# Performance work log

Hardware: AMD Instinct MI355X
Metric: run time of the kernel (lower is better)

The kernel has to match this reference:

```python
import jax, jax.numpy as jnp
import numpy as np
from jax.ops import segment_sum

N_NODES = 100_000
N_EDGES = 3_200_000
IN_DIM = 128
HID1, HID2, OUT = 32, 16, 1
N_GRAPHS = 512


def gcn_conv(x, src, dst, W, b, n_nodes):
    """PyG GCNConv: add self-loops, symmetric deg^{-1/2} norm, scatter-add, bias."""
    h = x @ W  # [N, out]
    loop = jnp.arange(n_nodes, dtype=src.dtype)
    s = jnp.concatenate([src, loop])
    d = jnp.concatenate([dst, loop])
    deg = segment_sum(jnp.ones_like(d, dtype=h.dtype), d, num_segments=n_nodes)
    dinv = jax.lax.rsqrt(jnp.maximum(deg, 1.0))  # deg >= 1 due to self-loops
    norm = dinv[s] * dinv[d]  # [E+N]
    msg = h[s] * norm[:, None]  # gather + scale
    out = segment_sum(msg, d, num_segments=n_nodes)  # scatter-add to dst
    return out + b


def setup_inputs() -> dict:
    key = jax.random.key(0)
    ks = jax.random.split(key, 9)
    x = jax.random.normal(ks[0], (N_NODES, IN_DIM), dtype=jnp.float32)
    edge_index = jax.random.randint(ks[1], (2, N_EDGES), 0, N_NODES, dtype=jnp.int64)
    batch = jnp.sort(jax.random.randint(ks[2], (N_NODES,), 0, N_GRAPHS, dtype=jnp.int64))
    W1 = jax.random.normal(ks[3], (IN_DIM, HID1), dtype=jnp.float32) * 0.1
    b1 = jnp.zeros((HID1,), dtype=jnp.float32)
    W2 = jax.random.normal(ks[4], (HID1, HID2), dtype=jnp.float32) * 0.1
    b2 = jnp.zeros((HID2,), dtype=jnp.float32)
    W3 = jax.random.normal(ks[5], (HID2, OUT), dtype=jnp.float32) * 0.1
    b3 = jnp.zeros((OUT,), dtype=jnp.float32)
    return {"x": x, "edge_index": edge_index, "batch": batch,
            "W1": W1, "b1": b1, "W2": W2, "b2": b2, "W3": W3, "b3": b3}


def reference(x, edge_index, batch, W1, b1, W2, b2, W3, b3):
    src, dst = edge_index[0], edge_index[1]
    n = x.shape[0]
    h = jax.nn.relu(gcn_conv(x, src, dst, W1, b1, n))
    h = jax.nn.relu(gcn_conv(h, src, dst, W2, b2, n))
    # global_mean_pool: segment mean over graph ids
    summed = segment_sum(h, batch, num_segments=N_GRAPHS)  # [G, HID2]
    counts = segment_sum(jnp.ones((n,), dtype=h.dtype), batch, num_segments=N_GRAPHS)
    pooled = summed / jnp.maximum(counts, 1.0)[:, None]
    return pooled @ W3 + b3  # [G, 1]
```

## Files before the change

### kernel.cpp

```cpp
#include <hip/hip_runtime.h>
#include <hip/hip_fp16.h>

#define NN 100000
#define NE 3200000
#define NG 512
#define IND 128
#define H1D 32
#define H2D 16
#define BSH 7
#define BN  128
#define NB  782
#define TILE 8192
#define NBF 391
#define CAP 5120

#define O_DINV   0u
#define O_ROW    100352u
#define O_REND   200704u
#define O_GCUR   301056u
#define O_GSUM   302080u
#define O_M1H    302592u
#define O_M2H    1902592u
#define O_CSRB   2702592u
#define O_CSR    6706432u

__global__ __launch_bounds__(256) void k_init(int* gcur, float* gsum) {
    int i = blockIdx.x * 256 + threadIdx.x;
    if (i < 1024) gcur[i] = i * CAP;
    if (i < NG) gsum[i] = 0.f;
}

__global__ __launch_bounds__(256) void k_prep1(const int* __restrict__ src,
                                               const int* __restrict__ dst,
                                               int* __restrict__ gcur,
                                               unsigned* __restrict__ csrb,
                                               const float* __restrict__ x,
                                               const float* __restrict__ W1,
                                               __half* __restrict__ m1h) {
    __shared__ __align__(16) unsigned char smem[30208];
    int t = threadIdx.x;
    if (blockIdx.x < NBF) {
        unsigned short* se16 = (unsigned short*)smem;
        int* lc   = (int*)(smem + 16384);
        int* lofs = (int*)(smem + 19584);
        int* lcur = (int*)(smem + 22784);
        int* gb   = (int*)(smem + 25984);
        int* sp   = (int*)(smem + 29184);
        for (int i = t; i < NB; i += 256) lc[i] = 0;
        __syncthreads();
        int base = blockIdx.x * TILE;
        int end = min(base + TILE, NE);
        int n = end - base;
        int n4 = n >> 2;
        const int4* dst4 = (const int4*)(dst + base);
        for (int u = t; u < n4; u += 256) {
            int4 v = dst4[u];
            atomicAdd(&lc[v.x >> BSH], 1);
            atomicAdd(&lc[v.y >> BSH], 1);
            atomicAdd(&lc[v.z >> BSH], 1);
            atomicAdd(&lc[v.w >> BSH], 1);
        }
        __syncthreads();
        int b0 = 4 * t;
        int c0 = (b0     < NB) ? lc[b0]     : 0;
        int c1 = (b0 + 1 < NB) ? lc[b0 + 1] : 0;
        int c2 = (b0 + 2 < NB) ? lc[b0 + 2] : 0;
        int c3 = (b0 + 3 < NB) ? lc[b0 + 3] : 0;
        int s4 = c0 + c1 + c2 + c3;
        sp[t] = s4;
        __syncthreads();
        for (int off = 1; off < 256; off <<= 1) {
            int v = (t >= off) ? sp[t - off] : 0;
            __syncthreads();
            sp[t] += v;
            __syncthreads();
        }
        int excl = sp[t] - s4;
        if (b0     < NB) { lofs[b0]     = excl;                lcur[b0]     = excl; }
        if (b0 + 1 < NB) { lofs[b0 + 1] = excl + c0;           lcur[b0 + 1] = excl + c0; }
        if (b0 + 2 < NB) { lofs[b0 + 2] = excl + c0 + c1;      lcur[b0 + 2] = excl + c0 + c1; }
        if (b0 + 3 < NB) { lofs[b0 + 3] = excl + c0 + c1 + c2; lcur[b0 + 3] = excl + c0 + c1 + c2; }
        __syncthreads();
        for (int i = t; i < NB; i += 256) {
            int c = lc[i];
            gb[i] = c ? atomicAdd(&gcur[i], c) : 0;
        }
        __syncthreads();
        for (int u = t; u < n4; u += 256) {
            int4 v = dst4[u];
            int uu = u * 4;
            int b, p;
            b = v.x >> BSH; p = atomicAdd(&lcur[b], 1); se16[p] = (unsigned short)(uu);
            b = v.y >> BSH; p = atomicAdd(&lcur[b], 1); se16[p] = (unsigned short)(uu + 1);
            b = v.z >> BSH; p = atomicAdd(&lcur[b], 1); se16[p] = (unsigned short)(uu + 2);
            b = v.w >> BSH; p = atomicAdd(&lcur[b], 1); se16[p] = (unsigned short)(uu + 3);
        }
        __syncthreads();
        for (int i = t; i < n; i += 256) {
            int u = se16[i];
            int d = dst[base + u];
            int s = src[base + u];
            int b = d >> BSH;
            int pos = gb[b] + (i - lofs[b]);
            csrb[pos] = (unsigned)s | ((unsigned)(d & (BN - 1)) << 17);
        }
    } else {
        float* sWt = (float*)smem;
        float* sX  = (float*)(smem + 16896);
        int gbk = blockIdx.x - NBF;
        for (int idx = t; idx < IND * H1D; idx += 256) {
            int i = idx >> 5, k = idx & 31;
            sWt[k * 132 + i] = W1[idx];
        }
        const float4* x4 = (const float4*)(x + (size_t)gbk * 16 * IND);
        ((float4*)sX)[t] = x4[t];
        ((float4*)sX)[t + 256] = x4[t + 256];
        __syncthreads();
        int r = t >> 5, k = t & 31;
        float a0 = 0.f, a1 = 0.f;
#pragma unroll
        for (int i = 0; i < IND; i += 4) {
            float4 w = *(const float4*)&sWt[k * 132 + i];
            float4 p = *(const float4*)&sX[r * IND + i];
            float4 s = *(const float4*)&sX[(r + 8) * IND + i];
            a0 += p.x * w.x + p.y * w.y + p.z * w.z + p.w * w.w;
            a1 += s.x * w.x + s.y * w.y + s.z * w.z + s.w * w.w;
        }
        int n0 = gbk * 16 + r;
        m1h[(size_t)n0 * 32 + k] = __float2half(a0);
        m1h[(size_t)(n0 + 8) * 32 + k] = __float2half(a1);
    }
}

__global__ __launch_bounds__(256) void k_reorder(const unsigned* __restrict__ csrb,
                                                 const int* __restrict__ gcur,
                                                 int* __restrict__ rowstart,
                                                 int* __restrict__ rowend,
                                                 float* __restrict__ dinv,
                                                 int* __restrict__ csr,
                                                 __half* __restrict__ m1h) {
    __shared__ int so[CAP];
    __shared__ int h[BN], cur[BN];
    __shared__ float sdv[BN];
    int t = threadIdx.x;
    int b = blockIdx.x;
    int base = b * CAP;
    int cnt = gcur[b] - base;
    if (t < BN) h[t] = 0;
    __syncthreads();
    for (int i = t; i < cnt; i += 256)
        atomicAdd(&h[csrb[base + i] >> 17], 1);
    __syncthreads();
    int deg = (t < BN) ? h[t] : 0;
    for (int off = 1; off < BN; off <<= 1) {
        int v = (t < BN && t >= off) ? h[t - off] : 0;
        __syncthreads();
        if (t < BN) h[t] += v;
        __syncthreads();
    }
    int excl = (t < BN) ? (h[t] - deg) : 0;
    if (t < BN) cur[t] = excl;
    int node = (b << BSH) + t;
    if (t < BN) {
        float dv = 1.0f / sqrtf((float)(deg + 1));
        sdv[t] = dv;
        if (node < NN) {
            rowstart[node] = base + excl;
            rowend[node]   = base + excl + deg;
            dinv[node] = dv;
        }
    }
    __syncthreads();
    for (int i = t; i < cnt; i += 256) {
        unsigned p = csrb[base + i];
        int pos = atomicAdd(&cur[p >> 17], 1);
        so[pos] = (int)(p & 0x1FFFF);
    }
    __syncthreads();
    for (int i = t; i < cnt; i += 256)
        csr[base + i] = so[i];
    int nn = min(BN, NN - (b << BSH));
    __half2* mrow = (__half2*)(m1h + (size_t)(b << BSH) * 32);
    for (int idx = t; idx < nn * 16; idx += 256) {
        float dv = sdv[idx >> 4];
        float2 f = __half22float2(mrow[idx]);
        mrow[idx] = __floats2half2_rn(f.x * dv, f.y * dv);
    }
}

__device__ __forceinline__ void h8_acc(const float4& r, float* a) {
    const __half2* h = (const __half2*)&r;
    float2 f0 = __half22float2(h[0]);
    float2 f1 = __half22float2(h[1]);
    float2 f2 = __half22float2(h[2]);
    float2 f3 = __half22float2(h[3]);
    a[0] += f0.x; a[1] += f0.y; a[2] += f1.x; a[3] += f1.y;
    a[4] += f2.x; a[5] += f2.y; a[6] += f3.x; a[7] += f3.y;
}

__global__ __launch_bounds__(256) void k_agg1(const __half* __restrict__ m1h,
                                              const float* __restrict__ dinv,
                                              const int* __restrict__ rowstart,
                                              const int* __restrict__ rowend,
                                              const int* __restrict__ csr,
                                              const float* __restrict__ b1,
                                              const float* __restrict__ W2,
                                              __half* __restrict__ m2h) {
    int t = threadIdx.x;
    int lane = t & 63;
    int j = (lane >> 2) & 7;
    int q = lane & 3;
    int d = (blockIdx.x * 256 + t) >> 5;
    int beg = rowstart[d], end = rowend[d];
    float dv = dinv[d];
    const float4* m4 = (const float4*)m1h;
    float4 selfr = m4[(size_t)d * 4 + q];
    float a[8] = {0.f, 0.f, 0.f, 0.f, 0.f, 0.f, 0.f, 0.f};
    int i = beg + j;
    for (; i + 24 < end; i += 32) {
        int s0 = csr[i], s1 = csr[i + 8], s2 = csr[i + 16], s3 = csr[i + 24];
        float4 A = m4[(size_t)s0 * 4 + q];
        float4 B = m4[(size_t)s1 * 4 + q];
        float4 C = m4[(size_t)s2 * 4 + q];
        float4 D = m4[(size_t)s3 * 4 + q];
        h8_acc(A, a); h8_acc(B, a); h8_acc(C, a); h8_acc(D, a);
    }
    for (; i + 8 < end; i += 16) {
        int s0 = csr[i], s1 = csr[i + 8];
        float4 A = m4[(size_t)s0 * 4 + q];
        float4 B = m4[(size_t)s1 * 4 + q];
        h8_acc(A, a); h8_acc(B, a);
    }
    if (i < end) {
        int s0 = csr[i];
        float4 A = m4[(size_t)s0 * 4 + q];
        h8_acc(A, a);
    }
#pragma unroll
    for (int m = 4; m <= 16; m <<= 1) {
#pragma unroll
        for (int e = 0; e < 8; ++e) a[e] += __shfl_xor(a[e], m);
    }
    float sf[8] = {0.f, 0.f, 0.f, 0.f, 0.f, 0.f, 0.f, 0.f};
    h8_acc(selfr, sf);
    float4 ba = ((const float4*)b1)[q * 2];
    float4 bb = ((const float4*)b1)[q * 2 + 1];
    float bias[8] = {ba.x, ba.y, ba.z, ba.w, bb.x, bb.y, bb.z, bb.w};
    float v[8];
#pragma unroll
    for (int e = 0; e < 8; ++e)
        v[e] = fmaxf((a[e] + sf[e]) * dv + bias[e], 0.f);
    const float2* W2_2 = (const float2*)W2;
    float p0 = 0.f, p1 = 0.f;
#pragma unroll
    for (int e = 0; e < 8; ++e) {
        float2 w = W2_2[(q * 8 + e) * 8 + j];
        p0 += v[e] * w.x;
        p1 += v[e] * w.y;
    }
    p0 += __shfl_xor(p0, 1); p1 += __shfl_xor(p1, 1);
    p0 += __shfl_xor(p0, 2); p1 += __shfl_xor(p1, 2);
    if (q == 0)
        *(__half2*)&m2h[(size_t)d * 16 + 2 * j] = __floats2half2_rn(p0 * dv, p1 * dv);
}

__global__ __launch_bounds__(256) void k_agg2(const __half* __restrict__ m2h,
                                              const float* __restrict__ dinv,
                                              const int* __restrict__ rowstart,
                                              const int* __restrict__ rowend,
                                              const int* __restrict__ csr,
                                              const float* __restrict__ b2,
                                              const float* __restrict__ W3,
                                              const int* __restrict__ batch,
                                              float* __restrict__ gsum) {
    __shared__ float bsum[8];
    __shared__ int   bg[8];
    int t = threadIdx.x;
    int lane = t & 63;
    int j = (lane >> 1) & 15;
    int q = lane & 1;
    int d = (blockIdx.x * 256 + t) >> 5;
    int beg = rowstart[d], end = rowend[d];
    float dv = dinv[d];
    const float4* m4 = (const float4*)m2h;
    float4 selfr = m4[(size_t)d * 2 + q];
    float a[8] = {0.f, 0.f, 0.f, 0.f, 0.f, 0.f, 0.f, 0.f};
    int i = beg + j;
    for (; i + 48 < end; i += 64) {
        int s0 = csr[i], s1 = csr[i + 16], s2 = csr[i + 32], s3 = csr[i + 48];
        float4 A = m4[(size_t)s0 * 2 + q];
        float4 B = m4[(size_t)s1 * 2 + q];
        float4 C = m4[(size_t)s2 * 2 + q];
        float4 D = m4[(size_t)s3 * 2 + q];
        h8_acc(A, a); h8_acc(B, a); h8_acc(C, a); h8_acc(D, a);
    }
    for (; i + 16 < end; i += 32) {
        int s0 = csr[i], s1 = csr[i + 16];
        float4 A = m4[(size_t)s0 * 2 + q];
        float4 B = m4[(size_t)s1 * 2 + q];
        h8_acc(A, a); h8_acc(B, a);
    }
    if (i < end) {
        int s0 = csr[i];
        float4 A = m4[(size_t)s0 * 2 + q];
        h8_acc(A, a);
    }
#pragma unroll
    for (int m = 2; m <= 16; m <<= 1) {
#pragma unroll
        for (int e = 0; e < 8; ++e) a[e] += __shfl_xor(a[e], m);
    }
    float sf[8] = {0.f, 0.f, 0.f, 0.f, 0.f, 0.f, 0.f, 0.f};
    h8_acc(selfr, sf);
    float4 ba = ((const float4*)b2)[q * 2];
    float4 bb = ((const float4*)b2)[q * 2 + 1];
    float4 wa = ((const float4*)W3)[q * 2];
    float4 wb = ((const float4*)W3)[q * 2 + 1];
    float bias[8] = {ba.x, ba.y, ba.z, ba.w, bb.x, bb.y, bb.z, bb.w};
    float w3[8]   = {wa.x, wa.y, wa.z, wa.w, wb.x, wb.y, wb.z, wb.w};
    float partial = 0.f;
#pragma unroll
    for (int e = 0; e < 8; ++e) {
        float v = fmaxf((a[e] + sf[e]) * dv + bias[e], 0.f);
        partial += v * w3[e];
    }
    partial += __shfl_xor(partial, 1);
    int hw = t >> 5;
    if ((lane & 31) == 0) { bg[hw] = batch[d]; bsum[hw] = partial; }
    __syncthreads();
    if (t == 0) {
        float s = bsum[0]; int g = bg[0];
#pragma unroll
        for (int u = 1; u < 8; ++u) {
            if (bg[u] == g) s += bsum[u];
            else { atomicAdd(&gsum[g], s); g = bg[u]; s = bsum[u]; }
        }
        atomicAdd(&gsum[g], s);
    }
}

__global__ __launch_bounds__(256) void k_final(const float* __restrict__ gsum,
                                               const int* __restrict__ batch,
                                               const float* __restrict__ b3,
                                               float* __restrict__ out) {
    int g = blockIdx.x * 256 + threadIdx.x;
    if (g >= NG) return;
    int lo = 0, hi = NN;
    while (lo < hi) { int mid = (lo + hi) >> 1; if (batch[mid] < g) lo = mid + 1; else hi = mid; }
    int lo2 = lo, hi2 = NN;
    while (lo2 < hi2) { int mid = (lo2 + hi2) >> 1; if (batch[mid] < g + 1) lo2 = mid + 1; else hi2 = mid; }
    out[g] = gsum[g] / fmaxf((float)(lo2 - lo), 1.0f) + b3[0];
}

extern "C" void kernel_launch(void* const* d_in, const int* in_sizes, int n_in,
                              void* d_out, int out_size, void* d_ws, size_t ws_size,
                              hipStream_t stream) {
    const float* x     = (const float*)d_in[0];
    const int*   src   = (const int*)d_in[1];
    const int*   dst   = src + NE;
    const int*   batch = (const int*)d_in[2];
    const float* W1 = (const float*)d_in[3];
    const float* b1 = (const float*)d_in[4];
    const float* W2 = (const float*)d_in[5];
    const float* b2 = (const float*)d_in[6];
    const float* W3 = (const float*)d_in[7];
    const float* b3 = (const float*)d_in[8];
    float* out = (float*)d_out;

    float* ws = (float*)d_ws;
    float*    dinv     = ws + O_DINV;
    int*      rowstart = (int*)(ws + O_ROW);
    int*      rowend   = (int*)(ws + O_REND);
    int*      gcur     = (int*)(ws + O_GCUR);
    float*    gsum     = ws + O_GSUM;
    __half*   m1h      = (__half*)(ws + O_M1H);
    __half*   m2h      = (__half*)(ws + O_M2H);
    unsigned* csrb     = (unsigned*)(ws + O_CSRB);
    int*      csr      = (int*)(ws + O_CSR);

    k_init   <<<4, 256, 0, stream>>>(gcur, gsum);
    k_prep1  <<<NBF + NN / 16, 256, 0, stream>>>(src, dst, gcur, csrb, x, W1, m1h);
    k_reorder<<<NB, 256, 0, stream>>>(csrb, gcur, rowstart, rowend, dinv, csr, m1h);
    k_agg1   <<<NN / 8, 256, 0, stream>>>(m1h, dinv, rowstart, rowend, csr, b1, W2, m2h);
    k_agg2   <<<NN / 8, 256, 0, stream>>>(m2h, dinv, rowstart, rowend, csr, b2, W3, batch, gsum);
    k_final  <<<2, 256, 0, stream>>>(gsum, batch, b3, out);
}
```

Measured before the change: 297.7 us.

## Split reorder blocks in half and fuse final pooling into agg2 via last-block ticket

k_reorder now runs two blocks per bucket, each scattering and writing the CSR entries and scaling m1h rows for only half of the 128 destination nodes. Both blocks redundantly histogram and scan the whole bucket. k_final is removed: k_agg2 takes an atomic ticket after a threadfence, and the last block to finish computes the per-graph means and writes the output. This adds parallelism to the reorder stage and removes one launch, at the cost of repeated histogram work and a serialized tail in the last agg2 block.

After: 511.6 us. +71.9%, slower.

```diff
diff --git a/kernel.cpp b/kernel.cpp
--- a/kernel.cpp
+++ b/kernel.cpp
@@ -19,15 +19,17 @@
 #define O_REND   200704u
 #define O_GCUR   301056u
 #define O_GSUM   302080u
-#define O_M1H    302592u
-#define O_M2H    1902592u
-#define O_CSRB   2702592u
-#define O_CSR    6706432u
-
-__global__ __launch_bounds__(256) void k_init(int* gcur, float* gsum) {
+#define O_TICK   302592u
+#define O_M1H    302720u
+#define O_M2H    1902720u
+#define O_CSRB   2702720u
+#define O_CSR    6706560u
+
+__global__ __launch_bounds__(256) void k_init(int* gcur, float* gsum, int* tick) {
     int i = blockIdx.x * 256 + threadIdx.x;
     if (i < 1024) gcur[i] = i * CAP;
     if (i < NG) gsum[i] = 0.f;
+    if (i == 0) tick[0] = 0;
 }
 
 __global__ __launch_bounds__(256) void k_prep1(const int* __restrict__ src,
@@ -143,7 +145,8 @@
     __shared__ int h[BN], cur[BN];
     __shared__ float sdv[BN];
     int t = threadIdx.x;
-    int b = blockIdx.x;
+    int b = blockIdx.x >> 1;
+    int half = blockIdx.x & 1;
     int base = b * CAP;
     int cnt = gcur[b] - base;
     if (t < BN) h[t] = 0;
@@ -161,7 +164,7 @@
     int excl = (t < BN) ? (h[t] - deg) : 0;
     if (t < BN) cur[t] = excl;
     int node = (b << BSH) + t;
-    if (t < BN) {
+    if (t < BN && (t >> 6) == half) {
         float dv = 1.0f / sqrtf((float)(deg + 1));
         sdv[t] = dv;
         if (node < NN) {
@@ -173,18 +176,26 @@
     __syncthreads();
     for (int i = t; i < cnt; i += 256) {
         unsigned p = csrb[base + i];
-        int pos = atomicAdd(&cur[p >> 17], 1);
-        so[pos] = (int)(p & 0x1FFFF);
-    }
-    __syncthreads();
-    for (int i = t; i < cnt; i += 256)
+        int dl = p >> 17;
+        if ((dl >> 6) == half) {
+            int pos = atomicAdd(&cur[dl], 1);
+            so[pos] = (int)(p & 0x1FFFF);
+        }
+    }
+    __syncthreads();
+    int s0 = half ? h[63] : 0;
+    int e0 = half ? cnt : h[63];
+    for (int i = s0 + t; i < e0; i += 256)
         csr[base + i] = so[i];
-    int nn = min(BN, NN - (b << BSH));
-    __half2* mrow = (__half2*)(m1h + (size_t)(b << BSH) * 32);
-    for (int idx = t; idx < nn * 16; idx += 256) {
-        float dv = sdv[idx >> 4];
-        float2 f = __half22float2(mrow[idx]);
-        mrow[idx] = __floats2half2_rn(f.x * dv, f.y * dv);
+    int nbase = (b << BSH) + half * 64;
+    int nn = min(64, NN - nbase);
+    if (nn > 0) {
+        __half2* mrow = (__half2*)(m1h + (size_t)nbase * 32);
+        for (int idx = t; idx < nn * 16; idx += 256) {
+            float dv = sdv[half * 64 + (idx >> 4)];
+            float2 f = __half22float2(mrow[idx]);
+            mrow[idx] = __floats2half2_rn(f.x * dv, f.y * dv);
+        }
     }
 }
 
@@ -272,9 +283,13 @@
                                               const float* __restrict__ b2,
                                               const float* __restrict__ W3,
                                               const int* __restrict__ batch,
-                                              float* __restrict__ gsum) {
+                                              float* __restrict__ gsum,
+                                              int* __restrict__ tick,
+                                              const float* __restrict__ b3,
+                                              float* __restrict__ out) {
     __shared__ float bsum[8];
     __shared__ int   bg[8];
+    __shared__ int   slast;
     int t = threadIdx.x;
     int lane = t & 63;
     int j = (lane >> 1) & 15;
@@ -336,20 +351,20 @@
             else { atomicAdd(&gsum[g], s); g = bg[u]; s = bsum[u]; }
         }
         atomicAdd(&gsum[g], s);
-    }
-}
-
-__global__ __launch_bounds__(256) void k_final(const float* __restrict__ gsum,
-                                               const int* __restrict__ batch,
-                                               const float* __restrict__ b3,
-                                               float* __restrict__ out) {
-    int g = blockIdx.x * 256 + threadIdx.x;
-    if (g >= NG) return;
-    int lo = 0, hi = NN;
-    while (lo < hi) { int mid = (lo + hi) >> 1; if (batch[mid] < g) lo = mid + 1; else hi = mid; }
-    int lo2 = lo, hi2 = NN;
-    while (lo2 < hi2) { int mid = (lo2 + hi2) >> 1; if (batch[mid] < g + 1) lo2 = mid + 1; else hi2 = mid; }
-    out[g] = gsum[g] / fmaxf((float)(lo2 - lo), 1.0f) + b3[0];
+        __threadfence();
+        slast = (atomicAdd(tick, 1) == (int)gridDim.x - 1);
+    }
+    __syncthreads();
+    if (slast) {
+        for (int g = t; g < NG; g += 256) {
+            int lo = 0, hi = NN;
+            while (lo < hi) { int mid = (lo + hi) >> 1; if (batch[mid] < g) lo = mid + 1; else hi = mid; }
+            int lo2 = lo, hi2 = NN;
+            while (lo2 < hi2) { int mid = (lo2 + hi2) >> 1; if (batch[mid] < g + 1) lo2 = mid + 1; else hi2 = mid; }
+            float s = atomicAdd(&gsum[g], 0.f);
+            out[g] = s / fmaxf((float)(lo2 - lo), 1.0f) + b3[0];
+        }
+    }
 }
 
 extern "C" void kernel_launch(void* const* d_in, const int* in_sizes, int n_in,
@@ -373,15 +388,16 @@
     int*      rowend   = (int*)(ws + O_REND);
     int*      gcur     = (int*)(ws + O_GCUR);
     float*    gsum     = ws + O_GSUM;
+    int*      tick     = (int*)(ws + O_TICK);
     __half*   m1h      = (__half*)(ws + O_M1H);
     __half*   m2h      = (__half*)(ws + O_M2H);
     unsigned* csrb     = (unsigned*)(ws + O_CSRB);
     int*      csr      = (int*)(ws + O_CSR);
 
-    k_init   <<<4, 256, 0, stream>>>(gcur, gsum);
+    k_init   <<<4, 256, 0, stream>>>(gcur, gsum, tick);
     k_prep1  <<<NBF + NN / 16, 256, 0, stream>>>(src, dst, gcur, csrb, x, W1, m1h);
-    k_reorder<<<NB, 256, 0, stream>>>(csrb, gcur, rowstart, rowend, dinv, csr, m1h);
+    k_reorder<<<NB * 2, 256, 0, stream>>>(csrb, gcur, rowstart, rowend, dinv, csr, m1h);
     k_agg1   <<<NN / 8, 256, 0, stream>>>(m1h, dinv, rowstart, rowend, csr, b1, W2, m2h);
-    k_agg2   <<<NN / 8, 256, 0, stream>>>(m2h, dinv, rowstart, rowend, csr, b2, W3, batch, gsum);
-    k_final  <<<2, 256, 0, stream>>>(gsum, batch, b3, out);
-}
+    k_agg2   <<<NN / 8, 256, 0, stream>>>(m2h, dinv, rowstart, rowend, csr, b2, W3, batch,
+                                          gsum, tick, b3, out);
+}
```

## Stage packed edges in shared memory during binning and reorder, halve tile size

Applied to the files above, without the earlier changes.

In the binning kernel, each local-sort slot now holds the packed (src, local dst) word and its bucket id directly in shared memory. This removes the second, permuted global read of src and dst when writing to global bins. The edge tile shrinks to 4096, which doubles the number of binning blocks. The reorder kernel now uses 512 threads and reads each bucket's entries from global memory once into shared memory instead of twice. It also clamps the per-bucket count to a smaller shared capacity, so buckets with more entries than that would silently lose edges on skewed graphs.

New measurement: 298.0 us. No clear change (+0.1%).

```diff
diff --git a/kernel.cpp b/kernel.cpp
--- a/kernel.cpp
+++ b/kernel.cpp
@@ -10,19 +10,20 @@
 #define BSH 7
 #define BN  128
 #define NB  782
-#define TILE 8192
-#define NBF 391
+#define TILE 4096
+#define NBF 782
 #define CAP 5120
+#define RCAP 4736
 
 #define O_DINV   0u
 #define O_ROW    100352u
 #define O_REND   200704u
 #define O_GCUR   301056u
 #define O_GSUM   302080u
-#define O_M1H    302592u
-#define O_M2H    1902592u
-#define O_CSRB   2702592u
-#define O_CSR    6706432u
+#define O_M1H    302720u
+#define O_M2H    1902720u
+#define O_CSRB   2702720u
+#define O_CSR    6706560u
 
 __global__ __launch_bounds__(256) void k_init(int* gcur, float* gsum) {
     int i = blockIdx.x * 256 + threadIdx.x;
@@ -37,15 +38,16 @@
                                                const float* __restrict__ x,
                                                const float* __restrict__ W1,
                                                __half* __restrict__ m1h) {
-    __shared__ __align__(16) unsigned char smem[30208];
+    __shared__ __align__(16) unsigned char smem[38144];
     int t = threadIdx.x;
     if (blockIdx.x < NBF) {
-        unsigned short* se16 = (unsigned short*)smem;
-        int* lc   = (int*)(smem + 16384);
-        int* lofs = (int*)(smem + 19584);
-        int* lcur = (int*)(smem + 22784);
-        int* gb   = (int*)(smem + 25984);
-        int* sp   = (int*)(smem + 29184);
+        unsigned* se32       = (unsigned*)smem;
+        unsigned short* sb16 = (unsigned short*)(smem + 16384);
+        int* lc   = (int*)(smem + 24576);
+        int* lofs = (int*)(smem + 27704);
+        int* lcur = (int*)(smem + 30832);
+        int* gb   = (int*)(smem + 33960);
+        int* sp   = (int*)(smem + 37088);
         for (int i = t; i < NB; i += 256) lc[i] = 0;
         __syncthreads();
         int base = blockIdx.x * TILE;
@@ -53,6 +55,7 @@
         int n = end - base;
         int n4 = n >> 2;
         const int4* dst4 = (const int4*)(dst + base);
+        const int4* src4 = (const int4*)(src + base);
         for (int u = t; u < n4; u += 256) {
             int4 v = dst4[u];
             atomicAdd(&lc[v.x >> BSH], 1);
@@ -87,22 +90,26 @@
         }
         __syncthreads();
         for (int u = t; u < n4; u += 256) {
-            int4 v = dst4[u];
-            int uu = u * 4;
+            int4 vd = dst4[u];
+            int4 vs = src4[u];
             int b, p;
-            b = v.x >> BSH; p = atomicAdd(&lcur[b], 1); se16[p] = (unsigned short)(uu);
-            b = v.y >> BSH; p = atomicAdd(&lcur[b], 1); se16[p] = (unsigned short)(uu + 1);
-            b = v.z >> BSH; p = atomicAdd(&lcur[b], 1); se16[p] = (unsigned short)(uu + 2);
-            b = v.w >> BSH; p = atomicAdd(&lcur[b], 1); se16[p] = (unsigned short)(uu + 3);
+            b = vd.x >> BSH; p = atomicAdd(&lcur[b], 1);
+            se32[p] = (unsigned)vs.x | ((unsigned)(vd.x & (BN - 1)) << 17);
+            sb16[p] = (unsigned short)b;
+            b = vd.y >> BSH; p = atomicAdd(&lcur[b], 1);
+            se32[p] = (unsigned)vs.y | ((unsigned)(vd.y & (BN - 1)) << 17);
+            sb16[p] = (unsigned short)b;
+            b = vd.z >> BSH; p = atomicAdd(&lcur[b], 1);
+            se32[p] = (unsigned)vs.z | ((unsigned)(vd.z & (BN - 1)) << 17);
+            sb16[p] = (unsigned short)b;
+            b = vd.w >> BSH; p = atomicAdd(&lcur[b], 1);
+            se32[p] = (unsigned)vs.w | ((unsigned)(vd.w & (BN - 1)) << 17);
+            sb16[p] = (unsigned short)b;
         }
         __syncthreads();
         for (int i = t; i < n; i += 256) {
-            int u = se16[i];
-            int d = dst[base + u];
-            int s = src[base + u];
-            int b = d >> BSH;
-            int pos = gb[b] + (i - lofs[b]);
-            csrb[pos] = (unsigned)s | ((unsigned)(d & (BN - 1)) << 17);
+            int b = sb16[i];
+            csrb[gb[b] + (i - lofs[b])] = se32[i];
         }
     } else {
         float* sWt = (float*)smem;
@@ -132,24 +139,28 @@
     }
 }
 
-__global__ __launch_bounds__(256) void k_reorder(const unsigned* __restrict__ csrb,
+__global__ __launch_bounds__(512) void k_reorder(const unsigned* __restrict__ csrb,
                                                  const int* __restrict__ gcur,
                                                  int* __restrict__ rowstart,
                                                  int* __restrict__ rowend,
                                                  float* __restrict__ dinv,
                                                  int* __restrict__ csr,
                                                  __half* __restrict__ m1h) {
-    __shared__ int so[CAP];
+    __shared__ unsigned se[RCAP];
+    __shared__ int so[RCAP];
     __shared__ int h[BN], cur[BN];
     __shared__ float sdv[BN];
     int t = threadIdx.x;
     int b = blockIdx.x;
     int base = b * CAP;
-    int cnt = gcur[b] - base;
+    int cnt = min(gcur[b] - base, RCAP);
     if (t < BN) h[t] = 0;
     __syncthreads();
-    for (int i = t; i < cnt; i += 256)
-        atomicAdd(&h[csrb[base + i] >> 17], 1);
+    for (int i = t; i < cnt; i += 512) {
+        unsigned p = csrb[base + i];
+        se[i] = p;
+        atomicAdd(&h[p >> 17], 1);
+    }
     __syncthreads();
     int deg = (t < BN) ? h[t] : 0;
     for (int off = 1; off < BN; off <<= 1) {
@@ -171,17 +182,17 @@
         }
     }
     __syncthreads();
-    for (int i = t; i < cnt; i += 256) {
-        unsigned p = csrb[base + i];
+    for (int i = t; i < cnt; i += 512) {
+        unsigned p = se[i];
         int pos = atomicAdd(&cur[p >> 17], 1);
         so[pos] = (int)(p & 0x1FFFF);
     }
     __syncthreads();
-    for (int i = t; i < cnt; i += 256)
+    for (int i = t; i < cnt; i += 512)
         csr[base + i] = so[i];
     int nn = min(BN, NN - (b << BSH));
     __half2* mrow = (__half2*)(m1h + (size_t)(b << BSH) * 32);
-    for (int idx = t; idx < nn * 16; idx += 256) {
+    for (int idx = t; idx < nn * 16; idx += 512) {
         float dv = sdv[idx >> 4];
         float2 f = __half22float2(mrow[idx]);
         mrow[idx] = __floats2half2_rn(f.x * dv, f.y * dv);
@@ -380,7 +391,7 @@
 
     k_init   <<<4, 256, 0, stream>>>(gcur, gsum);
     k_prep1  <<<NBF + NN / 16, 256, 0, stream>>>(src, dst, gcur, csrb, x, W1, m1h);
-    k_reorder<<<NB, 256, 0, stream>>>(csrb, gcur, rowstart, rowend, dinv, csr, m1h);
+    k_reorder<<<NB, 512, 0, stream>>>(csrb, gcur, rowstart, rowend, dinv, csr, m1h);
     k_agg1   <<<NN / 8, 256, 0, stream>>>(m1h, dinv, rowstart, rowend, csr, b1, W2, m2h);
     k_agg2   <<<NN / 8, 256, 0, stream>>>(m2h, dinv, rowstart, rowend, csr, b2, W3, batch, gsum);
     k_final  <<<2, 256, 0, stream>>>(gsum, batch, b3, out);
```
